# Kernel tuning notes

Hardware: AMD Instinct MI355X
Metric: run time of the kernel (lower is better)

Reference implementation:

```python
import jax, jax.numpy as jnp
import numpy as np

B, S, D, H = 2, 4096, 1024, 16
DK = D // H


def setup_inputs() -> dict:
    key = jax.random.key(0)
    ks = jax.random.split(key, 8)
    scale = 1.0 / np.sqrt(D)
    return {
        "q": jax.random.normal(ks[0], (B, S, D), dtype=jnp.float32),
        "k": jax.random.normal(ks[1], (B, S, D), dtype=jnp.float32),
        "v": jax.random.normal(ks[2], (B, S, D), dtype=jnp.float32),
        "mask": jax.random.randint(ks[3], (1, 1, S, S), 0, 2, dtype=jnp.int32),
        "w_q": jax.random.normal(ks[4], (D, D), dtype=jnp.float32) * scale,
        "w_k": jax.random.normal(ks[5], (D, D), dtype=jnp.float32) * scale,
        "w_v": jax.random.normal(ks[6], (D, D), dtype=jnp.float32) * scale,
        "w_o": jax.random.normal(ks[7], (D, D), dtype=jnp.float32) * scale,
    }


def reference(q, k, v, mask, w_q, w_k, w_v, w_o):
    # torch Linear(bias=False): y = x @ W.T
    def proj_split(x, w):
        y = jnp.einsum("bsd,ed->bse", x, w)  # [B,S,D]
        return y.reshape(x.shape[0], -1, H, DK).transpose(0, 2, 1, 3)  # [B,H,S,dk]

    Q = proj_split(q, w_q)
    K = proj_split(k, w_k)
    V = proj_split(v, w_v)

    scores = jnp.einsum("bhqd,bhkd->bhqk", Q, K) / jnp.sqrt(jnp.float32(DK))
    scores = jnp.where(mask == 0, jnp.float32(-1e9), scores)
    attn = jax.nn.softmax(scores, axis=-1)  # dropout p=0 -> identity
    ctx = jnp.einsum("bhqk,bhkd->bhqd", attn, V)  # [B,H,S,dk]
    ctx = ctx.transpose(0, 2, 1, 3).reshape(q.shape[0], -1, D)  # [B,S,D]
    return jnp.einsum("bsd,ed->bse", ctx, w_o)
```

## Files before the change

kernel.cpp:

```cpp
#include <hip/hip_runtime.h>
#include <math.h>
#include <stdint.h>

constexpr int B = 2, S = 4096, D = 1024, H = 16, DK = 64;
constexpr int M_TOT = B * S;

typedef __attribute__((ext_vector_type(8))) short bf16x8;
typedef __attribute__((ext_vector_type(4))) float f32x4;
typedef unsigned short u16;

__device__ inline u16 f2bf(float f) {
    uint32_t u = __builtin_bit_cast(uint32_t, f);
    u += 0x7fffu + ((u >> 16) & 1u);
    return (u16)(u >> 16);
}

__device__ inline u16 f2bf_hw(float f) {
    __bf16 h = (__bf16)f;
    return __builtin_bit_cast(u16, h);
}

__device__ inline void gl2lds16(const void* g, void* l) {
    __builtin_amdgcn_global_load_lds((const __attribute__((address_space(1))) void*)g,
                                     (__attribute__((address_space(3))) void*)l, 16, 0, 0);
}

__global__ __launch_bounds__(256) void conv_bf16(const float* __restrict__ s0, const float* __restrict__ s1,
                                                 const float* __restrict__ s2, const float* __restrict__ s3,
                                                 u16* __restrict__ d0, u16* __restrict__ d1,
                                                 u16* __restrict__ d2, u16* __restrict__ d3, int n) {
    const float* s; u16* d;
    switch (blockIdx.y) {
        case 0: s = s0; d = d0; break;
        case 1: s = s1; d = d1; break;
        case 2: s = s2; d = d2; break;
        default: s = s3; d = d3; break;
    }
    const int i = (blockIdx.x * 256 + threadIdx.x) * 4;
    if (i < n) {
        float4 v = *(const float4*)(s + i);
        ushort4 o;
        o.x = f2bf(v.x); o.y = f2bf(v.y); o.z = f2bf(v.z); o.w = f2bf(v.w);
        *(ushort4*)(d + i) = o;
    }
}

__global__ __launch_bounds__(256) void mask_pack(const int* __restrict__ m, uint32_t* __restrict__ out) {
    const int i = blockIdx.x * 256 + threadIdx.x;
    const int base = i * 32;
    uint32_t b = 0;
#pragma unroll
    for (int j = 0; j < 32; ++j) b |= (m[base + j] != 0 ? 1u : 0u) << j;
    out[i] = b;
}

template <typename OutT>
__global__ __launch_bounds__(256) void gemm_bt(const u16* __restrict__ X, const u16* __restrict__ Wm,
                                               OutT* __restrict__ Y, int M, int N, int K, float oscale) {
    __shared__ u16 As[128 * 64];
    __shared__ u16 Bs[128 * 64];
    const int tid = threadIdx.x;
    const int lane = tid & 63;
    const int wave = tid >> 6;
    const int l15 = lane & 15;
    const int quad = lane >> 4;
    const int i0 = blockIdx.x * 128;
    const int j0 = blockIdx.y * 128;
    const int wm = wave & 1, wn = wave >> 1;
    const int lr = lane >> 3;
    const int lc = (lane & 7) * 8;

    f32x4 zero = {0.f, 0.f, 0.f, 0.f};
    f32x4 acc[4][4];
#pragma unroll
    for (int a = 0; a < 4; ++a)
#pragma unroll
        for (int b2 = 0; b2 < 4; ++b2) acc[a][b2] = zero;

    for (int k0 = 0; k0 < K; k0 += 64) {
#pragma unroll
        for (int c = 0; c < 4; ++c) {
            const int ch = wave * 4 + c;
            const int row = ch * 8 + lr;
            gl2lds16(X + (size_t)(i0 + row) * K + k0 + lc, &As[ch * 512]);
            gl2lds16(Wm + (size_t)(j0 + row) * K + k0 + lc, &Bs[ch * 512]);
        }
        __syncthreads();
        bf16x8 af[4][2];
#pragma unroll
        for (int mt = 0; mt < 4; ++mt)
#pragma unroll
            for (int ks = 0; ks < 2; ++ks)
                af[mt][ks] = *(const bf16x8*)&As[(wm * 64 + mt * 16 + l15) * 64 + ks * 32 + quad * 8];
#pragma unroll
        for (int nt = 0; nt < 4; ++nt) {
#pragma unroll
            for (int ks = 0; ks < 2; ++ks) {
                bf16x8 bfr = *(const bf16x8*)&Bs[(wn * 64 + nt * 16 + l15) * 64 + ks * 32 + quad * 8];
#pragma unroll
                for (int mt = 0; mt < 4; ++mt)
                    acc[mt][nt] = __builtin_amdgcn_mfma_f32_16x16x32_bf16(af[mt][ks], bfr, acc[mt][nt], 0, 0, 0);
            }
        }
        __syncthreads();
    }
#pragma unroll
    for (int mt = 0; mt < 4; ++mt) {
#pragma unroll
        for (int r = 0; r < 4; ++r) {
            const int gi = i0 + wm * 64 + mt * 16 + quad * 4 + r;
#pragma unroll
            for (int nt = 0; nt < 4; ++nt) {
                const int gj = j0 + wn * 64 + nt * 16 + l15;
                const float v = acc[mt][nt][r] * oscale;
                if constexpr (sizeof(OutT) == 2) {
                    Y[(size_t)gi * N + gj] = (OutT)f2bf(v);
                } else {
                    Y[(size_t)gi * N + gj] = v;
                }
            }
        }
    }
}

__global__ __launch_bounds__(256) void attn_mfma(const u16* __restrict__ Qb, const u16* __restrict__ Kb,
                                                 const u16* __restrict__ Vt,
                                                 const uint64_t* __restrict__ mask64,
                                                 u16* __restrict__ ctx) {
    __shared__ u16 Ks[64 * 64];
    __shared__ u16 Vs[64 * 64];
    __shared__ u16 Ps[4][32 * 72];
    const int tid = threadIdx.x;
    const int lane = tid & 63;
    const int wave = tid >> 6;
    const int l15 = lane & 15;
    const int quad = lane >> 4;
    const int q0 = blockIdx.x * 128;
    const int bh = blockIdx.y;
    const int bb = bh >> 4, hh = bh & 15;
    const int mbase = bb * S;
    const int e0 = hh * DK;
    const int r7 = l15 & 7;

    const int srow = tid >> 2;
    const int scb = tid & 3;

    bf16x8 aq[2][2];
#pragma unroll
    for (int mi = 0; mi < 2; ++mi) {
        const u16* qrow = Qb + (size_t)(mbase + q0 + wave * 32 + mi * 16 + l15) * D + e0;
        aq[mi][0] = *(const bf16x8*)(qrow);
        aq[mi][0] = *(const bf16x8*)(qrow + quad * 8);
        aq[mi][1] = *(const bf16x8*)(qrow + 32 + quad * 8);
    }

    f32x4 O[2][4];
    f32x4 Ol[2];
#pragma unroll
    for (int mi = 0; mi < 2; ++mi) {
        Ol[mi] = (f32x4){0.f, 0.f, 0.f, 0.f};
#pragma unroll
        for (int dt = 0; dt < 4; ++dt) O[mi][dt] = (f32x4){0.f, 0.f, 0.f, 0.f};
    }

    bf16x8 ONES;
#pragma unroll
    for (int i = 0; i < 8; ++i) ONES[i] = (short)0x3F80;

    const uint64_t* mrow[2];
#pragma unroll
    for (int mi = 0; mi < 2; ++mi)
        mrow[mi] = mask64 + (size_t)(q0 + wave * 32 + mi * 16 + quad * 4) * (S / 64);

    for (int kt = 0; kt < S / 64; ++kt) {
        const int kb = kt * 64;
#pragma unroll
        for (int it = 0; it < 2; ++it) {
            const int cb = scb + it * 4;
            const int phys = cb ^ (srow & 7);
            const bf16x8 kvv = *(const bf16x8*)(Kb + (size_t)(mbase + kb + srow) * D + e0 + cb * 8);
            const bf16x8 vvv = *(const bf16x8*)(Vt + (size_t)(e0 + srow) * M_TOT + mbase + kb + cb * 8);
            *(bf16x8*)&Ks[srow * 64 + phys * 8] = kvv;
            *(bf16x8*)&Vs[srow * 64 + phys * 8] = vvv;
        }
        __syncthreads();

        bf16x8 kf[4][2];
#pragma unroll
        for (int nt = 0; nt < 4; ++nt) {
            kf[nt][0] = *(const bf16x8*)&Ks[(nt * 16 + l15) * 64 + (quad ^ r7) * 8];
            kf[nt][1] = *(const bf16x8*)&Ks[(nt * 16 + l15) * 64 + ((quad + 4) ^ r7) * 8];
        }

#pragma unroll
        for (int mi = 0; mi < 2; ++mi) {
            f32x4 sa[4];
#pragma unroll
            for (int nt = 0; nt < 4; ++nt) {
                f32x4 c = {0.f, 0.f, 0.f, 0.f};
                c = __builtin_amdgcn_mfma_f32_16x16x32_bf16(aq[mi][0], kf[nt][0], c, 0, 0, 0);
                c = __builtin_amdgcn_mfma_f32_16x16x32_bf16(aq[mi][1], kf[nt][1], c, 0, 0, 0);
                sa[nt] = c;
            }
            uint32_t mlo[4], mhi[4];
#pragma unroll
            for (int r = 0; r < 4; ++r) {
                const uint64_t sh = mrow[mi][(size_t)r * (S / 64) + kt] >> l15;
                mlo[r] = (uint32_t)sh;
                mhi[r] = (uint32_t)(sh >> 32);
            }
            u16* pw = &Ps[wave][mi * 16 * 72];
#pragma unroll
            for (int nt = 0; nt < 4; ++nt) {
#pragma unroll
                for (int r = 0; r < 4; ++r) {
                    const uint32_t w32 = (nt < 2) ? mlo[r] : mhi[r];
                    const uint32_t bit = (w32 >> ((nt & 1) * 16)) & 1u;
                    float p = __builtin_amdgcn_exp2f(sa[nt][r]);
                    p = bit ? p : 0.f;
                    pw[(quad * 4 + r) * 72 + nt * 16 + l15] = f2bf_hw(p);
                }
            }
        }

        bf16x8 ap[2][2];
#pragma unroll
        for (int mi = 0; mi < 2; ++mi)
#pragma unroll
            for (int ks = 0; ks < 2; ++ks)
                ap[mi][ks] = *(const bf16x8*)&Ps[wave][(mi * 16 + l15) * 72 + ks * 32 + quad * 8];

#pragma unroll
        for (int mi = 0; mi < 2; ++mi) {
            Ol[mi] = __builtin_amdgcn_mfma_f32_16x16x32_bf16(ap[mi][0], ONES, Ol[mi], 0, 0, 0);
            Ol[mi] = __builtin_amdgcn_mfma_f32_16x16x32_bf16(ap[mi][1], ONES, Ol[mi], 0, 0, 0);
        }
#pragma unroll
        for (int dt = 0; dt < 4; ++dt) {
            const bf16x8 bv0 = *(const bf16x8*)&Vs[(dt * 16 + l15) * 64 + (quad ^ r7) * 8];
            const bf16x8 bv1 = *(const bf16x8*)&Vs[(dt * 16 + l15) * 64 + ((quad + 4) ^ r7) * 8];
#pragma unroll
            for (int mi = 0; mi < 2; ++mi) {
                O[mi][dt] = __builtin_amdgcn_mfma_f32_16x16x32_bf16(ap[mi][0], bv0, O[mi][dt], 0, 0, 0);
                O[mi][dt] = __builtin_amdgcn_mfma_f32_16x16x32_bf16(ap[mi][1], bv1, O[mi][dt], 0, 0, 0);
            }
        }
        __syncthreads();
    }

#pragma unroll
    for (int mi = 0; mi < 2; ++mi) {
#pragma unroll
        for (int r = 0; r < 4; ++r) {
            const float inv = 1.f / Ol[mi][r];
            const int gm = mbase + q0 + wave * 32 + mi * 16 + quad * 4 + r;
#pragma unroll
            for (int dt = 0; dt < 4; ++dt)
                ctx[(size_t)gm * D + e0 + dt * 16 + l15] = f2bf(O[mi][dt][r] * inv);
        }
    }
}

extern "C" void kernel_launch(void* const* d_in, const int* in_sizes, int n_in,
                              void* d_out, int out_size, void* d_ws, size_t ws_size,
                              hipStream_t stream) {
    (void)in_sizes; (void)n_in; (void)out_size; (void)ws_size;
    const float* q = (const float*)d_in[0];
    const float* k = (const float*)d_in[1];
    const float* v = (const float*)d_in[2];
    const int* msk = (const int*)d_in[3];
    const float* w_q = (const float*)d_in[4];
    const float* w_k = (const float*)d_in[5];
    const float* w_v = (const float*)d_in[6];
    const float* w_o = (const float*)d_in[7];
    float* out = (float*)d_out;

    const size_t MB = 1u << 20;
    char* w = (char*)d_ws;
    u16* qb   = (u16*)(w + 0 * MB);
    u16* kb   = (u16*)(w + 16 * MB);
    u16* vb   = (u16*)(w + 32 * MB);
    u16* wqb  = (u16*)(w + 48 * MB);
    u16* wkb  = (u16*)(w + 50 * MB);
    u16* wvb  = (u16*)(w + 52 * MB);
    u16* wob  = (u16*)(w + 54 * MB);
    uint64_t* maskb = (uint64_t*)(w + 56 * MB);
    u16* Qf   = (u16*)(w + 58 * MB);
    u16* Kf   = (u16*)(w + 74 * MB);
    u16* Vtf  = (u16*)(w + 90 * MB);
    u16* ctxb = (u16*)(w + 106 * MB);

    const float SCL2 = 0.18033688011112042f;

    dim3 blk(256);
    conv_bf16<<<dim3(8192, 3), blk, 0, stream>>>(q, k, v, q, qb, kb, vb, qb, M_TOT * D);
    conv_bf16<<<dim3(1024, 4), blk, 0, stream>>>(w_q, w_k, w_v, w_o, wqb, wkb, wvb, wob, D * D);
    mask_pack<<<dim3(S * S / 32 / 256), blk, 0, stream>>>(msk, (uint32_t*)maskb);

    gemm_bt<u16><<<dim3(M_TOT / 128, D / 128), blk, 0, stream>>>(qb, wqb, Qf, M_TOT, D, D, SCL2);
    gemm_bt<u16><<<dim3(M_TOT / 128, D / 128), blk, 0, stream>>>(kb, wkb, Kf, M_TOT, D, D, 1.0f);
    gemm_bt<u16><<<dim3(D / 128, M_TOT / 128), blk, 0, stream>>>(wvb, vb, Vtf, D, M_TOT, D, 1.0f);

    attn_mfma<<<dim3(S / 128, B * H), blk, 0, stream>>>(Qf, Kf, Vtf, maskb, ctxb);

    gemm_bt<float><<<dim3(M_TOT / 128, D / 128), blk, 0, stream>>>(ctxb, wob, out, M_TOT, D, D, 1.0f);
}
```

Before: 596.6 us.

## Keep softmax probabilities in registers by transposing score MFMA and permuting V tile

The score MFMA operands are swapped so each lane holds a row of P in the layout the PV MFMA expects. This removes the per-wave LDS round trip for P (scalar stores, a read-back and the Ps buffer). The V tile is loaded with a matching k-permutation using two 8-byte loads. The mask is now read as one 64-bit word per row and lane instead of four, at the cost of narrower global V loads.

```diff
diff --git a/kernel.cpp b/kernel.cpp
--- a/kernel.cpp
+++ b/kernel.cpp
@@ -7,6 +7,7 @@
 
 typedef __attribute__((ext_vector_type(8))) short bf16x8;
 typedef __attribute__((ext_vector_type(4))) float f32x4;
+typedef __attribute__((ext_vector_type(4))) uint32_t u32x4;
 typedef unsigned short u16;
 
 __device__ inline u16 f2bf(float f) {
@@ -129,7 +130,6 @@
                                                  u16* __restrict__ ctx) {
     __shared__ u16 Ks[64 * 64];
     __shared__ u16 Vs[64 * 64];
-    __shared__ u16 Ps[4][32 * 72];
     const int tid = threadIdx.x;
     const int lane = tid & 63;
     const int wave = tid >> 6;
@@ -149,7 +149,6 @@
 #pragma unroll
     for (int mi = 0; mi < 2; ++mi) {
         const u16* qrow = Qb + (size_t)(mbase + q0 + wave * 32 + mi * 16 + l15) * D + e0;
-        aq[mi][0] = *(const bf16x8*)(qrow);
         aq[mi][0] = *(const bf16x8*)(qrow + quad * 8);
         aq[mi][1] = *(const bf16x8*)(qrow + 32 + quad * 8);
     }
@@ -170,7 +169,7 @@
     const uint64_t* mrow[2];
 #pragma unroll
     for (int mi = 0; mi < 2; ++mi)
-        mrow[mi] = mask64 + (size_t)(q0 + wave * 32 + mi * 16 + quad * 4) * (S / 64);
+        mrow[mi] = mask64 + (size_t)(q0 + wave * 32 + mi * 16 + l15) * (S / 64);
 
     for (int kt = 0; kt < S / 64; ++kt) {
         const int kb = kt * 64;
@@ -179,9 +178,13 @@
             const int cb = scb + it * 4;
             const int phys = cb ^ (srow & 7);
             const bf16x8 kvv = *(const bf16x8*)(Kb + (size_t)(mbase + kb + srow) * D + e0 + cb * 8);
-            const bf16x8 vvv = *(const bf16x8*)(Vt + (size_t)(e0 + srow) * M_TOT + mbase + kb + cb * 8);
             *(bf16x8*)&Ks[srow * 64 + phys * 8] = kvv;
-            *(bf16x8*)&Vs[srow * 64 + phys * 8] = vvv;
+            const int k0v = 32 * (cb >> 2) + 4 * (cb & 3);
+            const u16* vsrc = Vt + (size_t)(e0 + srow) * M_TOT + mbase + kb + k0v;
+            const uint64_t va = *(const uint64_t*)(vsrc);
+            const uint64_t vb = *(const uint64_t*)(vsrc + 16);
+            *(uint64_t*)&Vs[srow * 64 + phys * 8] = va;
+            *(uint64_t*)&Vs[srow * 64 + phys * 8 + 4] = vb;
         }
         __syncthreads();
 
@@ -192,43 +195,38 @@
             kf[nt][1] = *(const bf16x8*)&Ks[(nt * 16 + l15) * 64 + ((quad + 4) ^ r7) * 8];
         }
 
+        bf16x8 ap[2][2];
 #pragma unroll
         for (int mi = 0; mi < 2; ++mi) {
             f32x4 sa[4];
 #pragma unroll
             for (int nt = 0; nt < 4; ++nt) {
                 f32x4 c = {0.f, 0.f, 0.f, 0.f};
-                c = __builtin_amdgcn_mfma_f32_16x16x32_bf16(aq[mi][0], kf[nt][0], c, 0, 0, 0);
-                c = __builtin_amdgcn_mfma_f32_16x16x32_bf16(aq[mi][1], kf[nt][1], c, 0, 0, 0);
+                c = __builtin_amdgcn_mfma_f32_16x16x32_bf16(kf[nt][0], aq[mi][0], c, 0, 0, 0);
+                c = __builtin_amdgcn_mfma_f32_16x16x32_bf16(kf[nt][1], aq[mi][1], c, 0, 0, 0);
                 sa[nt] = c;
             }
-            uint32_t mlo[4], mhi[4];
-#pragma unroll
-            for (int r = 0; r < 4; ++r) {
-                const uint64_t sh = mrow[mi][(size_t)r * (S / 64) + kt] >> l15;
-                mlo[r] = (uint32_t)sh;
-                mhi[r] = (uint32_t)(sh >> 32);
-            }
-            u16* pw = &Ps[wave][mi * 16 * 72];
+            const uint64_t mw = mrow[mi][kt];
+            const uint32_t mlo = (uint32_t)(mw >> (quad * 4));
+            const uint32_t mhi = (uint32_t)(mw >> (quad * 4 + 32));
+            uint32_t pk[4][2];
 #pragma unroll
             for (int nt = 0; nt < 4; ++nt) {
+                const uint32_t mx = (nt < 2) ? mlo : mhi;
+                float p[4];
 #pragma unroll
                 for (int r = 0; r < 4; ++r) {
-                    const uint32_t w32 = (nt < 2) ? mlo[r] : mhi[r];
-                    const uint32_t bit = (w32 >> ((nt & 1) * 16)) & 1u;
-                    float p = __builtin_amdgcn_exp2f(sa[nt][r]);
-                    p = bit ? p : 0.f;
-                    pw[(quad * 4 + r) * 72 + nt * 16 + l15] = f2bf_hw(p);
+                    const float e = __builtin_amdgcn_exp2f(sa[nt][r]);
+                    p[r] = ((mx >> ((nt & 1) * 16 + r)) & 1u) ? e : 0.f;
                 }
-            }
-        }
-
-        bf16x8 ap[2][2];
-#pragma unroll
-        for (int mi = 0; mi < 2; ++mi)
-#pragma unroll
-            for (int ks = 0; ks < 2; ++ks)
-                ap[mi][ks] = *(const bf16x8*)&Ps[wave][(mi * 16 + l15) * 72 + ks * 32 + quad * 8];
+                pk[nt][0] = (uint32_t)f2bf_hw(p[0]) | ((uint32_t)f2bf_hw(p[1]) << 16);
+                pk[nt][1] = (uint32_t)f2bf_hw(p[2]) | ((uint32_t)f2bf_hw(p[3]) << 16);
+            }
+            const u32x4 w0 = {pk[0][0], pk[0][1], pk[1][0], pk[1][1]};
+            const u32x4 w1 = {pk[2][0], pk[2][1], pk[3][0], pk[3][1]};
+            ap[mi][0] = __builtin_bit_cast(bf16x8, w0);
+            ap[mi][1] = __builtin_bit_cast(bf16x8, w1);
+        }
 
 #pragma unroll
         for (int mi = 0; mi < 2; ++mi) {
```

Result: faster. 535.3 us (-10.3%).
